# Kernel optimization log

Measured on AMD Instinct MI355X. Metric: run time of the kernel, lower is better.

The kernel has to match this reference:

```python
import jax, jax.numpy as jnp
import numpy as np

LAYER_SPECS = [(2, 4, 1), (2, 4, 1), (1, 4, 1), (1, 4, 1)]
SKIPS = [(k - s) * d for (s, k, d) in LAYER_SPECS]  # (ksz-stride)*dilation
C = 80  # encoder channels


def _conv1d(x, w, b, stride, dilation):
    # x: (N, Cin, L), w: (Cout, Cin, K)
    out = jax.lax.conv_general_dilated(
        x, w, window_strides=(stride,), padding='VALID',
        rhs_dilation=(dilation,), dimension_numbers=('NCH', 'OIH', 'NCH'))
    return out + b[None, :, None]


def _encoder(x, w_wide, b_wide, w_1x1, b_1x1, w_f0, b_f0, w_f1, b_f1):
    # x: (N, T, 80) -> (N, T', 80)
    x = jnp.transpose(x, (0, 2, 1))  # (N, 80, T)
    for i, ((stride, ksz, dil), skip) in enumerate(zip(LAYER_SPECS, SKIPS)):
        x1 = _conv1d(x, w_wide[i], b_wide[i], stride, dil)  # (N, 2C, L')
        a, g = jnp.split(x1, 2, axis=1)
        x2 = jnp.tanh(a) * jax.nn.sigmoid(g)                # gated activation
        x3 = _conv1d(x2, w_1x1[i], b_1x1[i], 1, 1)          # (N, C, L')
        if i == 0:
            x = x3
        else:
            T3 = x3.shape[2]
            # residual: strided slice of previous x, take last of each stride group
            res = x[:, :, skip:skip + T3 * stride].reshape(x.shape[0], C, T3, stride)[:, :, :, -1]
            x = x3 + res
    x = _conv1d(jax.nn.relu(_conv1d(x, w_f0, b_f0, 1, 1)), w_f1, b_f1, 1, 1)
    return jnp.transpose(x, (0, 2, 1))  # (N, T', 80)


def setup_inputs() -> dict:
    key = jax.random.key(0)
    ks = jax.random.split(key, 10)
    N, Ts, Tq = 16, 8192, 2048
    return {
        'search': jax.random.normal(ks[0], (N, Ts, 80), dtype=jnp.float32),
        'query': jax.random.normal(ks[1], (N, Tq, 80), dtype=jnp.float32),
        'w_wide': jax.random.normal(ks[2], (4, 160, 80, 4), dtype=jnp.float32) * 0.02,
        'b_wide': jnp.zeros((4, 160), dtype=jnp.float32),
        'w_1x1': jax.random.normal(ks[3], (4, 80, 80, 1), dtype=jnp.float32) * 0.05,
        'b_1x1': jnp.zeros((4, 80), dtype=jnp.float32),
        'w_f0': jax.random.normal(ks[4], (80, 80, 1), dtype=jnp.float32) * 0.05,
        'b_f0': jnp.zeros((80,), dtype=jnp.float32),
        'w_f1': jax.random.normal(ks[5], (80, 80, 1), dtype=jnp.float32) * 0.05,
        'b_f1': jax.random.normal(ks[6], (80,), dtype=jnp.float32) * 0.05,
        'embedding': jax.random.normal(ks[7], (1, 512, 80), dtype=jnp.float32) * 0.001,
        'w_lin': jax.random.normal(ks[8], (2, 80), dtype=jnp.float32) * 0.05,
        'b_lin': jnp.zeros((2,), dtype=jnp.float32),
    }


def reference(search, query, w_wide, b_wide, w_1x1, b_1x1,
              w_f0, b_f0, w_f1, b_f1, embedding, w_lin, b_lin):
    enc_s = _encoder(search, w_wide, b_wide, w_1x1, b_1x1, w_f0, b_f0, w_f1, b_f1)
    enc_q = _encoder(query, w_wide, b_wide, w_1x1, b_1x1, w_f0, b_f0, w_f1, b_f1)

    # ---- VectorQuant (no normalize): nearest-codeword lookup + straight-through ----
    x = enc_s[:, :, None, :]                  # (N, T, 1, V)
    N, T, nc, V = x.shape
    n_classes = embedding.shape[1]
    x1 = x.reshape(N * T, nc, V)              # (NT, 1, V)
    # squared-distance via expansion: argmin identical to argmin of L2 norm
    x2 = jnp.sum(x1 * x1, axis=-1, keepdims=True)          # (NT, 1, 1)
    e2 = jnp.sum(embedding * embedding, axis=-1)[None]     # (1, 1, K)
    xe = jnp.einsum('ncv,ckv->nck', x1, embedding)         # (NT, 1, K)
    idx = jnp.argmin(x2 - 2.0 * xe + e2, axis=2)           # (NT, 1)
    offset = jnp.arange(nc) * n_classes
    flat = embedding.reshape(-1, V)
    output = flat[(idx + offset[None, :]).reshape(-1)].reshape(x.shape)
    out0 = jax.lax.stop_gradient(output - x) + x           # straight-through
    discrete = out0[:, :, 0, :]               # (N, Ts', V)

    # ---- align query to search length, classify, max-pool over time ----
    sf = discrete.shape[1] // enc_q.shape[1]
    q = jnp.tile(enc_q, (1, sf, 1))
    pad = discrete.shape[1] - q.shape[1]
    q = jnp.pad(q, ((0, 0), (0, pad), (0, 0)))
    pred = jnp.tanh((q + discrete) @ w_lin.T + b_lin)      # (N, Ts', 2)
    return jnp.max(pred, axis=1)                           # (N, 2)
```

## Files before the change

### kernel.cpp

```cpp
#include <hip/hip_runtime.h>
#include <math.h>


#define NBATCH 16

typedef __attribute__((ext_vector_type(8))) short s16x8;
typedef __attribute__((ext_vector_type(4))) float f32x4;

__device__ __forceinline__ float fast_sigmoid(float x){ return 1.0f/(1.0f+__expf(-x)); }
__device__ __forceinline__ float fast_tanh(float x){ return 2.0f/(1.0f+__expf(-2.0f*x))-1.0f; }
__device__ __forceinline__ unsigned short f2bf(float f){
    unsigned int u = __float_as_uint(f);
    return (unsigned short)((u + 0x7FFFu + ((u >> 16) & 1u)) >> 16);
}

__global__ __launch_bounds__(256) void pack_all(
    const float* __restrict__ w_wide, const float* __restrict__ w_1x1,
    const float* __restrict__ wf0,    const float* __restrict__ wf1,
    const float* __restrict__ emb,
    unsigned short* __restrict__ WW, unsigned short* __restrict__ W1,
    unsigned short* __restrict__ F0, unsigned short* __restrict__ F1,
    unsigned short* __restrict__ EM, float* __restrict__ e2o)
{
    int i = blockIdx.x * 256 + threadIdx.x;
    if (i < 204800) {
        int l = i / 51200, r = i % 51200, oc = r / 320, k = r % 320;
        int j = k / 80, ic = k % 80;
        WW[i] = f2bf(w_wide[l * 51200 + oc * 320 + ic * 4 + j]);
    } else if (i < 235520) {
        int idx = i - 204800, l = idx / 7680, r = idx % 7680, oc = r / 96, k = r % 96;
        W1[idx] = (k < 80) ? f2bf(w_1x1[l * 6400 + oc * 80 + k]) : (unsigned short)0;
    } else if (i < 243200) {
        int idx = i - 235520, oc = idx / 96, k = idx % 96;
        F0[idx] = (k < 80) ? f2bf(wf0[oc * 80 + k]) : (unsigned short)0;
    } else if (i < 250880) {
        int idx = i - 243200, oc = idx / 96, k = idx % 96;
        F1[idx] = (k < 80) ? f2bf(wf1[oc * 80 + k]) : (unsigned short)0;
    } else if (i < 291840) {
        EM[i - 250880] = f2bf(emb[i - 250880]);
    } else if (i < 292352) {
        int e = i - 291840;
        float s = 0.f;
        for (int k = 0; k < 80; ++k) { float v = emb[e * 80 + k]; s = fmaf(v, v, s); }
        e2o[e] = s;
    }
}

template<int S, bool HAS_RES, bool FINAL>
__global__ __launch_bounds__(320, 3) void enc_layer(
    const float* __restrict__ xS, const float* __restrict__ xQ,
    const unsigned short* __restrict__ ww,  const float* __restrict__ wb,
    const unsigned short* __restrict__ w1p, const float* __restrict__ b1,
    const unsigned short* __restrict__ f0p, const float* __restrict__ bf0,
    const unsigned short* __restrict__ f1p, const float* __restrict__ bf1,
    float* __restrict__ outS, float* __restrict__ outQ,
    int TinS, int ToutS, int TinQ, int ToutQ, int nbS)
{
    constexpr int P    = 63 * S + 4;
    constexpr int HALF = (S == 2) ? 65 : 67;
    constexpr int NPAR = (S == 2) ? 2 : 1;
    constexpr int XS_SH = NPAR * HALF * 88;
    constexpr int GS_SH = 64 * 104;
    constexpr int R1   = (XS_SH > GS_SH) ? XS_SH : GS_SH;
    __shared__ unsigned short smem[R1];
    unsigned short* xs = smem;
    unsigned short* gs = smem;

    const int tid  = threadIdx.x;
    const int wave = tid >> 6;
    const int lane = tid & 63;
    const int m    = lane & 15;
    const int quad = lane >> 4;
    const int n_   = blockIdx.y;

    const float* x; float* out; int T_in, T_out, bx;
    if ((int)blockIdx.x < nbS) { x = xS; out = outS; T_in = TinS; T_out = ToutS; bx = blockIdx.x; }
    else                       { x = xQ; out = outQ; T_in = TinQ; T_out = ToutQ; bx = blockIdx.x - nbS; }
    const int t0 = bx * 64;
    const long base_in = (long)n_ * T_in * 80;

    for (int u = tid; u < P * 20; u += 320) {
        int pos = u / 20, c4 = u % 20;
        int tp = t0 * S + pos; if (tp > T_in - 1) tp = T_in - 1;
        float4 v = *(const float4*)(x + base_in + (long)tp * 80 + c4 * 4);
        int row = (S == 2) ? (pos >> 1) : pos;
        int par = (S == 2) ? (pos & 1) : 0;
        int o = (par * HALF + row) * 88 + c4 * 4;
        unsigned int s0 = (unsigned int)f2bf(v.x) | ((unsigned int)f2bf(v.y) << 16);
        unsigned int s1 = (unsigned int)f2bf(v.z) | ((unsigned int)f2bf(v.w) << 16);
        *(uint2*)&xs[o] = make_uint2(s0, s1);
    }

    const int quad8 = quad * 8;
    const unsigned short* wa_base = ww + (long)(wave * 16 + m) * 320 + quad8;
    const unsigned short* wg_base = ww + (long)((wave + 5) * 16 + m) * 320 + quad8;
    auto ldB = [&](const unsigned short* b, int kk) { return *(const s16x8*)(b + kk * 32); };

    s16x8 baP[3], bgP[3];
    baP[0] = ldB(wa_base, 0); bgP[0] = ldB(wg_base, 0);
    baP[1] = ldB(wa_base, 1); bgP[1] = ldB(wg_base, 1);

    f32x4 acc_a[4], acc_g[4];
#pragma unroll
    for (int mt = 0; mt < 4; ++mt) {
        acc_a[mt] = (f32x4){0.f, 0.f, 0.f, 0.f};
        acc_g[mt] = (f32x4){0.f, 0.f, 0.f, 0.f};
    }

    __syncthreads();

#pragma unroll
    for (int kk = 0; kk < 10; ++kk) {
        if (kk + 2 < 10) {
            baP[(kk + 2) % 3] = ldB(wa_base, kk + 2);
            bgP[(kk + 2) % 3] = ldB(wg_base, kk + 2);
        }
        const int kq = kk * 32 + quad8;
        const int j  = (kq >= 240) ? 3 : ((kq >= 160) ? 2 : ((kq >= 80) ? 1 : 0));
        const int ic0 = kq - j * 80;
        int xb;
        if (S == 2) xb = ((j & 1) * HALF + (j >> 1)) * 88 + ic0;
        else        xb = j * 88 + ic0;
        s16x8 a[4];
#pragma unroll
        for (int mt = 0; mt < 4; ++mt)
            a[mt] = *(const s16x8*)&xs[xb + (mt * 16 + m) * 88];
        s16x8 ba = baP[kk % 3], bg = bgP[kk % 3];
#pragma unroll
        for (int mt = 0; mt < 4; ++mt) {
            acc_a[mt] = __builtin_amdgcn_mfma_f32_16x16x32_bf16(a[mt], ba, acc_a[mt], 0, 0, 0);
            acc_g[mt] = __builtin_amdgcn_mfma_f32_16x16x32_bf16(a[mt], bg, acc_g[mt], 0, 0, 0);
        }
    }

    __syncthreads();
    const float ba_b = wb[wave * 16 + m];
    const float bg_b = wb[80 + wave * 16 + m];
#pragma unroll
    for (int mt = 0; mt < 4; ++mt)
#pragma unroll
        for (int r = 0; r < 4; ++r) {
            float av = acc_a[mt][r] + ba_b;
            float gv = acc_g[mt][r] + bg_b;
            gs[(mt * 16 + quad * 4 + r) * 104 + wave * 16 + m] =
                f2bf(fast_tanh(av) * fast_sigmoid(gv));
        }
    const uint4 z4 = make_uint4(0u, 0u, 0u, 0u);
    for (int u = tid; u < 128; u += 320)
        *(uint4*)&gs[(u >> 1) * 104 + 80 + (u & 1) * 8] = z4;
    __syncthreads();

    auto mm96 = [&](const unsigned short* Wp, f32x4 (&o)[4]) {
        const unsigned short* wb1 = Wp + (long)(wave * 16 + m) * 96 + quad8;
        s16x8 b0 = *(const s16x8*)(wb1);
        s16x8 b1f = *(const s16x8*)(wb1 + 32);
        s16x8 b2 = *(const s16x8*)(wb1 + 64);
#pragma unroll
        for (int mt = 0; mt < 4; ++mt) o[mt] = (f32x4){0.f, 0.f, 0.f, 0.f};
#pragma unroll
        for (int kb = 0; kb < 3; ++kb) {
            s16x8 b = (kb == 0) ? b0 : ((kb == 1) ? b1f : b2);
#pragma unroll
            for (int mt = 0; mt < 4; ++mt) {
                s16x8 ag = *(const s16x8*)&gs[(mt * 16 + m) * 104 + kb * 32 + quad8];
                o[mt] = __builtin_amdgcn_mfma_f32_16x16x32_bf16(ag, b, o[mt], 0, 0, 0);
            }
        }
    };

    f32x4 a1[4];
    mm96(w1p, a1);

    const long base_out = (long)n_ * T_out * 80;
    const int c = wave * 16 + m;
    if (!FINAL) {
        const float b1c = b1[c];
#pragma unroll
        for (int mt = 0; mt < 4; ++mt)
#pragma unroll
            for (int r = 0; r < 4; ++r) {
                int tg = t0 + mt * 16 + quad * 4 + r;
                if (tg < T_out) {
                    float v = a1[mt][r] + b1c;
                    if (HAS_RES)
                        v += x[base_in + (long)(3 + (long)tg * S) * 80 + c];
                    out[base_out + (long)tg * 80 + c] = v;
                }
            }
    } else {
        const float b1c = b1[c];
        float x3[4][4];
#pragma unroll
        for (int mt = 0; mt < 4; ++mt)
#pragma unroll
            for (int r = 0; r < 4; ++r) {
                int tg = t0 + mt * 16 + quad * 4 + r;
                int tc = (tg < T_out) ? tg : (T_out - 1);
                float v = a1[mt][r] + b1c;
                if (HAS_RES)
                    v += x[base_in + (long)(3 + (long)tc * S) * 80 + c];
                x3[mt][r] = v;
            }
        __syncthreads();
#pragma unroll
        for (int mt = 0; mt < 4; ++mt)
#pragma unroll
            for (int r = 0; r < 4; ++r)
                gs[(mt * 16 + quad * 4 + r) * 104 + c] = f2bf(x3[mt][r]);
        __syncthreads();
        f32x4 a2[4];
        mm96(f0p, a2);
        const float bf0c = bf0[c];
        __syncthreads();
#pragma unroll
        for (int mt = 0; mt < 4; ++mt)
#pragma unroll
            for (int r = 0; r < 4; ++r)
                gs[(mt * 16 + quad * 4 + r) * 104 + c] =
                    f2bf(fmaxf(a2[mt][r] + bf0c, 0.f));
        __syncthreads();
        f32x4 a3[4];
        mm96(f1p, a3);
        const float bf1c = bf1[c];
#pragma unroll
        for (int mt = 0; mt < 4; ++mt)
#pragma unroll
            for (int r = 0; r < 4; ++r) {
                int tg = t0 + mt * 16 + quad * 4 + r;
                if (tg < T_out)
                    out[base_out + (long)tg * 80 + c] = a3[mt][r] + bf1c;
            }
    }
}

__global__ __launch_bounds__(256, 2) void vq_mfma(
    const float* __restrict__ enc_s, const float* __restrict__ enc_q,
    const unsigned short* __restrict__ embp, const float* __restrict__ emb,
    const float* __restrict__ e2v,
    const float* __restrict__ w_lin, const float* __restrict__ b_lin,
    float* __restrict__ pred)
{
    __shared__ unsigned short xs[64 * 104];
    __shared__ unsigned short es[128 * 104];
    const uint4 z4 = make_uint4(0u, 0u, 0u, 0u);

    const int tid  = threadIdx.x;
    const int wave = tid >> 6;
    const int lane = tid & 63;
    const int m    = lane & 15;
    const int quad = lane >> 4;
    const int n    = blockIdx.y;
    const int t0   = blockIdx.x * 64;

    for (int u = tid; u < 64 * 20; u += 256) {
        int row = u / 20, c4 = u % 20;
        int t = t0 + row; if (t > 2039) t = 2039;
        float4 v = *(const float4*)(enc_s + ((long)n * 2040 + t) * 80 + c4 * 4);
        unsigned int s0 = (unsigned int)f2bf(v.x) | ((unsigned int)f2bf(v.y) << 16);
        unsigned int s1 = (unsigned int)f2bf(v.z) | ((unsigned int)f2bf(v.w) << 16);
        *(uint2*)&xs[row * 104 + c4 * 4] = make_uint2(s0, s1);
    }
    for (int u = tid; u < 128; u += 256)
        *(uint4*)&xs[(u >> 1) * 104 + 80 + (u & 1) * 8] = z4;
    __syncthreads();

    s16x8 af[3];
#pragma unroll
    for (int kb = 0; kb < 3; ++kb)
        af[kb] = *(const s16x8*)&xs[(wave * 16 + m) * 104 + kb * 32 + quad * 8];

    float best[4]; int bi[4];
#pragma unroll
    for (int r = 0; r < 4; ++r) { best[r] = 1e30f; bi[r] = 0; }

    for (int ch = 0; ch < 4; ++ch) {
        const int c0 = ch * 128;
        __syncthreads();
        for (int u = tid; u < 128 * 12; u += 256) {
            int el = u / 12, seg = u % 12;
            uint4 v = z4;
            if (seg < 10) v = *(const uint4*)(embp + (long)(c0 + el) * 80 + seg * 8);
            *(uint4*)&es[el * 104 + seg * 8] = v;
        }
        __syncthreads();

        f32x4 acc[8];
#pragma unroll
        for (int nt = 0; nt < 8; ++nt) acc[nt] = (f32x4){0.f, 0.f, 0.f, 0.f};
#pragma unroll
        for (int kb = 0; kb < 3; ++kb) {
            const int k0 = kb * 32 + quad * 8;
#pragma unroll
            for (int nt = 0; nt < 8; ++nt) {
                s16x8 b = *(const s16x8*)&es[(nt * 16 + m) * 104 + k0];
                acc[nt] = __builtin_amdgcn_mfma_f32_16x16x32_bf16(af[kb], b, acc[nt], 0, 0, 0);
            }
        }
#pragma unroll
        for (int nt = 0; nt < 8; ++nt) {
            const int e = c0 + nt * 16 + m;
            const float e2x = e2v[e];
#pragma unroll
            for (int r = 0; r < 4; ++r) {
                float s = fmaf(-2.0f, acc[nt][r], e2x);
                if (s < best[r]) { best[r] = s; bi[r] = e; }
            }
        }
    }

    __syncthreads();
    float* rb = (float*)es;
    int*   ri = (int*)es + 1088;
#pragma unroll
    for (int r = 0; r < 4; ++r) {
        int tl = wave * 16 + quad * 4 + r;
        rb[tl * 17 + m] = best[r];
        ri[tl * 17 + m] = bi[r];
    }
    __syncthreads();

    if (tid < 64) {
        const int t = t0 + tid;
        float b = rb[tid * 17]; int ix = ri[tid * 17];
#pragma unroll
        for (int j = 1; j < 16; ++j) {
            float v = rb[tid * 17 + j]; int iv = ri[tid * 17 + j];
            if (v < b || (v == b && iv < ix)) { b = v; ix = iv; }
        }
        if (t < 2040) {
            const float4* ev = (const float4*)(emb + (long)ix * 80);
            const bool hasq = (t < 2016);
            const float4* qv = hasq
                ? (const float4*)(enc_q + ((long)n * 504 + (t % 504)) * 80) : nullptr;
            float p0 = b_lin[0], p1 = b_lin[1];
#pragma unroll
            for (int i = 0; i < 20; ++i) {
                float4 e4 = ev[i];
                float4 q4 = hasq ? qv[i] : make_float4(0.f, 0.f, 0.f, 0.f);
                float4 w0 = *(const float4*)(w_lin + 4 * i);
                float4 w1 = *(const float4*)(w_lin + 80 + 4 * i);
                float sx = e4.x + q4.x, sy = e4.y + q4.y;
                float sz = e4.z + q4.z, sw = e4.w + q4.w;
                p0 = fmaf(sx, w0.x, p0); p1 = fmaf(sx, w1.x, p1);
                p0 = fmaf(sy, w0.y, p0); p1 = fmaf(sy, w1.y, p1);
                p0 = fmaf(sz, w0.z, p0); p1 = fmaf(sz, w1.z, p1);
                p0 = fmaf(sw, w0.w, p0); p1 = fmaf(sw, w1.w, p1);
            }
            long o = ((long)n * 2040 + t) * 2;
            pred[o]     = fast_tanh(p0);
            pred[o + 1] = fast_tanh(p1);
        }
    }
}

__global__ __launch_bounds__(256) void max_red(const float* __restrict__ pred,
                                               float* __restrict__ out)
{
    __shared__ float s0[256], s1[256];
    const int n = blockIdx.x, tid = threadIdx.x;
    float m0 = -1e30f, m1 = -1e30f;
    for (int t = tid; t < 2040; t += 256) {
        long o = ((long)n * 2040 + t) * 2;
        m0 = fmaxf(m0, pred[o]);
        m1 = fmaxf(m1, pred[o + 1]);
    }
    s0[tid] = m0; s1[tid] = m1;
    __syncthreads();
    for (int st = 128; st > 0; st >>= 1) {
        if (tid < st) {
            s0[tid] = fmaxf(s0[tid], s0[tid + st]);
            s1[tid] = fmaxf(s1[tid], s1[tid + st]);
        }
        __syncthreads();
    }
    if (tid == 0) { out[n * 2] = s0[0]; out[n * 2 + 1] = s1[0]; }
}

extern "C" void kernel_launch(void* const* d_in, const int* in_sizes, int n_in,
                              void* d_out, int out_size, void* d_ws, size_t ws_size,
                              hipStream_t stream)
{
    const float* search = (const float*)d_in[0];
    const float* query  = (const float*)d_in[1];
    const float* w_wide = (const float*)d_in[2];
    const float* b_wide = (const float*)d_in[3];
    const float* w_1x1  = (const float*)d_in[4];
    const float* b_1x1  = (const float*)d_in[5];
    const float* w_f0   = (const float*)d_in[6];
    const float* b_f0   = (const float*)d_in[7];
    const float* w_f1   = (const float*)d_in[8];
    const float* b_f1   = (const float*)d_in[9];
    const float* emb    = (const float*)d_in[10];
    const float* w_lin  = (const float*)d_in[11];
    const float* b_lin  = (const float*)d_in[12];
    float* out = (float*)d_out;
    float* ws  = (float*)d_ws;

    float* A  = ws;
    float* B  = A  + 5241600;
    float* C  = B  + 2618880;
    float* QA = C  + 2618880;
    float* QB = QA + 1309440;
    float* QC = QB + 652800;
    unsigned short* WWp = (unsigned short*)(QC + 652800);
    unsigned short* W1p = WWp + 204800;
    unsigned short* F0p = W1p + 30720;
    unsigned short* F1p = F0p + 7680;
    unsigned short* EMp = F1p + 7680;
    float* e2b = (float*)(EMp + 40960);

    const dim3 blk(320);
    auto nb = [](int T) { return (T + 63) / 64; };

    pack_all<<<dim3(1142), dim3(256), 0, stream>>>(w_wide, w_1x1, w_f0, w_f1, emb,
                                                   WWp, W1p, F0p, F1p, EMp, e2b);

    enc_layer<2, false, false><<<dim3(nb(4095) + nb(1023), NBATCH), blk, 0, stream>>>(
        search, query, WWp, b_wide, W1p, b_1x1, nullptr, nullptr, nullptr, nullptr,
        A, QA, 8192, 4095, 2048, 1023, nb(4095));
    enc_layer<2, true, false><<<dim3(nb(2046) + nb(510), NBATCH), blk, 0, stream>>>(
        A, QA, WWp + 51200, b_wide + 160, W1p + 7680, b_1x1 + 80,
        nullptr, nullptr, nullptr, nullptr,
        B, QB, 4095, 2046, 1023, 510, nb(2046));
    enc_layer<1, true, false><<<dim3(nb(2043) + nb(507), NBATCH), blk, 0, stream>>>(
        B, QB, WWp + 102400, b_wide + 320, W1p + 15360, b_1x1 + 160,
        nullptr, nullptr, nullptr, nullptr,
        C, QC, 2046, 2043, 510, 507, nb(2043));
    enc_layer<1, true, true><<<dim3(nb(2040) + nb(504), NBATCH), blk, 0, stream>>>(
        C, QC, WWp + 153600, b_wide + 480, W1p + 23040, b_1x1 + 240,
        F0p, b_f0, F1p, b_f1,
        B, QB, 2043, 2040, 507, 504, nb(2040));

    vq_mfma<<<dim3(32, NBATCH), dim3(256), 0, stream>>>(B, QB, EMp, emb, e2b,
                                                        w_lin, b_lin, C);
    max_red<<<dim3(NBATCH), dim3(256), 0, stream>>>(C, out);
}
```

Before: 233.3 us.

## Halve encoder time tile, raise occupancy, split smem buffers to drop barriers

The encoder layer kernel now processes 32 output timesteps per block instead of 64, halving accumulators and shared memory so launch bounds can request 6 blocks per CU. Input staging loads are issued into registers before the weight prefetch and written to LDS afterward, overlapping global latency. Separate xs/gsA/gsB buffers replace the aliased smem, removing several __syncthreads. The cost is more halo recomputation per block (conv overlap), more blocks, and less weight reuse per block.

```diff
diff --git a/kernel.cpp b/kernel.cpp
--- a/kernel.cpp
+++ b/kernel.cpp
@@ -47,7 +47,7 @@
 }
 
 template<int S, bool HAS_RES, bool FINAL>
-__global__ __launch_bounds__(320, 3) void enc_layer(
+__global__ __launch_bounds__(320, 6) void enc_layer(
     const float* __restrict__ xS, const float* __restrict__ xQ,
     const unsigned short* __restrict__ ww,  const float* __restrict__ wb,
     const unsigned short* __restrict__ w1p, const float* __restrict__ b1,
@@ -56,15 +56,17 @@
     float* __restrict__ outS, float* __restrict__ outQ,
     int TinS, int ToutS, int TinQ, int ToutQ, int nbS)
 {
-    constexpr int P    = 63 * S + 4;
-    constexpr int HALF = (S == 2) ? 65 : 67;
-    constexpr int NPAR = (S == 2) ? 2 : 1;
-    constexpr int XS_SH = NPAR * HALF * 88;
-    constexpr int GS_SH = 64 * 104;
-    constexpr int R1   = (XS_SH > GS_SH) ? XS_SH : GS_SH;
-    __shared__ unsigned short smem[R1];
-    unsigned short* xs = smem;
-    unsigned short* gs = smem;
+    constexpr int TILE = 32;
+    constexpr int MT   = 2;
+    constexpr int P    = (TILE - 1) * S + 4;
+    constexpr int HALF = (S == 2) ? (P / 2) : P;
+    constexpr int NEL  = P * 20;
+    constexpr int NST  = (NEL + 319) / 320;
+    constexpr int NPARY = (S == 2) ? 2 : 1;
+
+    __shared__ __attribute__((aligned(16))) unsigned short xs[NPARY * HALF * 88];
+    __shared__ __attribute__((aligned(16))) unsigned short gsA[TILE * 104];
+    __shared__ __attribute__((aligned(16))) unsigned short gsB[FINAL ? TILE * 104 : 8];
 
     const int tid  = threadIdx.x;
     const int wave = tid >> 6;
@@ -76,33 +78,45 @@
     const float* x; float* out; int T_in, T_out, bx;
     if ((int)blockIdx.x < nbS) { x = xS; out = outS; T_in = TinS; T_out = ToutS; bx = blockIdx.x; }
     else                       { x = xQ; out = outQ; T_in = TinQ; T_out = ToutQ; bx = blockIdx.x - nbS; }
-    const int t0 = bx * 64;
+    const int t0 = bx * TILE;
     const long base_in = (long)n_ * T_in * 80;
-
-    for (int u = tid; u < P * 20; u += 320) {
-        int pos = u / 20, c4 = u % 20;
-        int tp = t0 * S + pos; if (tp > T_in - 1) tp = T_in - 1;
-        float4 v = *(const float4*)(x + base_in + (long)tp * 80 + c4 * 4);
-        int row = (S == 2) ? (pos >> 1) : pos;
-        int par = (S == 2) ? (pos & 1) : 0;
-        int o = (par * HALF + row) * 88 + c4 * 4;
-        unsigned int s0 = (unsigned int)f2bf(v.x) | ((unsigned int)f2bf(v.y) << 16);
-        unsigned int s1 = (unsigned int)f2bf(v.z) | ((unsigned int)f2bf(v.w) << 16);
-        *(uint2*)&xs[o] = make_uint2(s0, s1);
-    }
 
     const int quad8 = quad * 8;
     const unsigned short* wa_base = ww + (long)(wave * 16 + m) * 320 + quad8;
     const unsigned short* wg_base = ww + (long)((wave + 5) * 16 + m) * 320 + quad8;
     auto ldB = [&](const unsigned short* b, int kk) { return *(const s16x8*)(b + kk * 32); };
 
+    float4 vst[NST]; int odx[NST]; bool okw[NST];
+#pragma unroll
+    for (int it = 0; it < NST; ++it) {
+        int u = tid + it * 320;
+        okw[it] = (u < NEL);
+        if (u >= NEL) u = NEL - 1;
+        int pos = u / 20, c4 = u % 20;
+        int tp = t0 * S + pos; if (tp > T_in - 1) tp = T_in - 1;
+        vst[it] = *(const float4*)(x + base_in + (long)tp * 80 + c4 * 4);
+        int row = (S == 2) ? (pos >> 1) : pos;
+        int par = (S == 2) ? (pos & 1) : 0;
+        odx[it] = (par * HALF + row) * 88 + c4 * 4;
+    }
+
     s16x8 baP[3], bgP[3];
     baP[0] = ldB(wa_base, 0); bgP[0] = ldB(wg_base, 0);
     baP[1] = ldB(wa_base, 1); bgP[1] = ldB(wg_base, 1);
 
-    f32x4 acc_a[4], acc_g[4];
-#pragma unroll
-    for (int mt = 0; mt < 4; ++mt) {
+#pragma unroll
+    for (int it = 0; it < NST; ++it) {
+        if (okw[it]) {
+            float4 v = vst[it];
+            unsigned int s0 = (unsigned int)f2bf(v.x) | ((unsigned int)f2bf(v.y) << 16);
+            unsigned int s1 = (unsigned int)f2bf(v.z) | ((unsigned int)f2bf(v.w) << 16);
+            *(uint2*)&xs[odx[it]] = make_uint2(s0, s1);
+        }
+    }
+
+    f32x4 acc_a[MT], acc_g[MT];
+#pragma unroll
+    for (int mt = 0; mt < MT; ++mt) {
         acc_a[mt] = (f32x4){0.f, 0.f, 0.f, 0.f};
         acc_g[mt] = (f32x4){0.f, 0.f, 0.f, 0.f};
     }
@@ -121,62 +135,67 @@
         int xb;
         if (S == 2) xb = ((j & 1) * HALF + (j >> 1)) * 88 + ic0;
         else        xb = j * 88 + ic0;
-        s16x8 a[4];
-#pragma unroll
-        for (int mt = 0; mt < 4; ++mt)
+        s16x8 a[MT];
+#pragma unroll
+        for (int mt = 0; mt < MT; ++mt)
             a[mt] = *(const s16x8*)&xs[xb + (mt * 16 + m) * 88];
         s16x8 ba = baP[kk % 3], bg = bgP[kk % 3];
 #pragma unroll
-        for (int mt = 0; mt < 4; ++mt) {
+        for (int mt = 0; mt < MT; ++mt) {
             acc_a[mt] = __builtin_amdgcn_mfma_f32_16x16x32_bf16(a[mt], ba, acc_a[mt], 0, 0, 0);
             acc_g[mt] = __builtin_amdgcn_mfma_f32_16x16x32_bf16(a[mt], bg, acc_g[mt], 0, 0, 0);
         }
     }
 
-    __syncthreads();
     const float ba_b = wb[wave * 16 + m];
     const float bg_b = wb[80 + wave * 16 + m];
 #pragma unroll
-    for (int mt = 0; mt < 4; ++mt)
+    for (int mt = 0; mt < MT; ++mt)
 #pragma unroll
         for (int r = 0; r < 4; ++r) {
             float av = acc_a[mt][r] + ba_b;
             float gv = acc_g[mt][r] + bg_b;
-            gs[(mt * 16 + quad * 4 + r) * 104 + wave * 16 + m] =
+            gsA[(mt * 16 + quad * 4 + r) * 104 + wave * 16 + m] =
                 f2bf(fast_tanh(av) * fast_sigmoid(gv));
         }
     const uint4 z4 = make_uint4(0u, 0u, 0u, 0u);
-    for (int u = tid; u < 128; u += 320)
-        *(uint4*)&gs[(u >> 1) * 104 + 80 + (u & 1) * 8] = z4;
-    __syncthreads();
-
-    auto mm96 = [&](const unsigned short* Wp, f32x4 (&o)[4]) {
+    {
+        constexpr int NPAD = FINAL ? 128 : 64;
+        for (int u = tid; u < NPAD; u += 320) {
+            unsigned short* g = (u < 64) ? gsA : gsB;
+            int v = u & 63;
+            *(uint4*)&g[(v >> 1) * 104 + 80 + (v & 1) * 8] = z4;
+        }
+    }
+    __syncthreads();
+
+    auto mm96 = [&](const unsigned short* Wp, const unsigned short* g, f32x4 (&o)[MT]) {
         const unsigned short* wb1 = Wp + (long)(wave * 16 + m) * 96 + quad8;
-        s16x8 b0 = *(const s16x8*)(wb1);
+        s16x8 b0  = *(const s16x8*)(wb1);
         s16x8 b1f = *(const s16x8*)(wb1 + 32);
-        s16x8 b2 = *(const s16x8*)(wb1 + 64);
-#pragma unroll
-        for (int mt = 0; mt < 4; ++mt) o[mt] = (f32x4){0.f, 0.f, 0.f, 0.f};
+        s16x8 b2  = *(const s16x8*)(wb1 + 64);
+#pragma unroll
+        for (int mt = 0; mt < MT; ++mt) o[mt] = (f32x4){0.f, 0.f, 0.f, 0.f};
 #pragma unroll
         for (int kb = 0; kb < 3; ++kb) {
             s16x8 b = (kb == 0) ? b0 : ((kb == 1) ? b1f : b2);
 #pragma unroll
-            for (int mt = 0; mt < 4; ++mt) {
-                s16x8 ag = *(const s16x8*)&gs[(mt * 16 + m) * 104 + kb * 32 + quad8];
+            for (int mt = 0; mt < MT; ++mt) {
+                s16x8 ag = *(const s16x8*)&g[(mt * 16 + m) * 104 + kb * 32 + quad8];
                 o[mt] = __builtin_amdgcn_mfma_f32_16x16x32_bf16(ag, b, o[mt], 0, 0, 0);
             }
         }
     };
 
-    f32x4 a1[4];
-    mm96(w1p, a1);
+    f32x4 a1[MT];
+    mm96(w1p, gsA, a1);
 
     const long base_out = (long)n_ * T_out * 80;
     const int c = wave * 16 + m;
     if (!FINAL) {
         const float b1c = b1[c];
 #pragma unroll
-        for (int mt = 0; mt < 4; ++mt)
+        for (int mt = 0; mt < MT; ++mt)
 #pragma unroll
             for (int r = 0; r < 4; ++r) {
                 int tg = t0 + mt * 16 + quad * 4 + r;
@@ -189,9 +208,9 @@
             }
     } else {
         const float b1c = b1[c];
-        float x3[4][4];
-#pragma unroll
-        for (int mt = 0; mt < 4; ++mt)
+        float x3[MT][4];
+#pragma unroll
+        for (int mt = 0; mt < MT; ++mt)
 #pragma unroll
             for (int r = 0; r < 4; ++r) {
                 int tg = t0 + mt * 16 + quad * 4 + r;
@@ -201,29 +220,27 @@
                     v += x[base_in + (long)(3 + (long)tc * S) * 80 + c];
                 x3[mt][r] = v;
             }
+#pragma unroll
+        for (int mt = 0; mt < MT; ++mt)
+#pragma unroll
+            for (int r = 0; r < 4; ++r)
+                gsB[(mt * 16 + quad * 4 + r) * 104 + c] = f2bf(x3[mt][r]);
         __syncthreads();
-#pragma unroll
-        for (int mt = 0; mt < 4; ++mt)
+        f32x4 a2[MT];
+        mm96(f0p, gsB, a2);
+        const float bf0c = bf0[c];
+#pragma unroll
+        for (int mt = 0; mt < MT; ++mt)
 #pragma unroll
             for (int r = 0; r < 4; ++r)
-                gs[(mt * 16 + quad * 4 + r) * 104 + c] = f2bf(x3[mt][r]);
-        __syncthreads();
-        f32x4 a2[4];
-        mm96(f0p, a2);
-        const float bf0c = bf0[c];
-        __syncthreads();
-#pragma unroll
-        for (int mt = 0; mt < 4; ++mt)
-#pragma unroll
-            for (int r = 0; r < 4; ++r)
-                gs[(mt * 16 + quad * 4 + r) * 104 + c] =
+                gsA[(mt * 16 + quad * 4 + r) * 104 + c] =
                     f2bf(fmaxf(a2[mt][r] + bf0c, 0.f));
         __syncthreads();
-        f32x4 a3[4];
-        mm96(f1p, a3);
+        f32x4 a3[MT];
+        mm96(f1p, gsA, a3);
         const float bf1c = bf1[c];
 #pragma unroll
-        for (int mt = 0; mt < 4; ++mt)
+        for (int mt = 0; mt < MT; ++mt)
 #pragma unroll
             for (int r = 0; r < 4; ++r) {
                 int tg = t0 + mt * 16 + quad * 4 + r;
@@ -410,7 +427,7 @@
     float* e2b = (float*)(EMp + 40960);
 
     const dim3 blk(320);
-    auto nb = [](int T) { return (T + 63) / 64; };
+    auto nb = [](int T) { return (T + 31) / 32; };
 
     pack_all<<<dim3(1142), dim3(256), 0, stream>>>(w_wide, w_1x1, w_f0, w_f1, emb,
                                                    WWp, W1p, F0p, F1p, EMp, e2b);
```

New measurement: 240.8 us. +3.2%, slower.
